# Optimization experiments

Measured on AMD Instinct MI355X. Metric: run time of the kernel, lower is better.

## Reference

```python
import jax, jax.numpy as jnp
import numpy as np

B, S, D, K, F = 4, 2048, 1024, 4, 4096
C_COEF = 8.0  # RG-LRU gating exponent from Griffin paper
EPS = 1e-6


def setup_inputs() -> dict:
    key = jax.random.key(0)
    ks = jax.random.split(key, 12)
    def n(k, shape, scale=1.0):
        return jax.random.normal(k, shape, dtype=jnp.float32) * scale
    sd = 1.0 / np.sqrt(D)
    return {
        "x": n(ks[0], (B, S, D)),
        "velocity": n(ks[1], (B, S, D), 0.1),
        "pre_norm_w": jnp.ones((D,), jnp.float32),
        "conv_kernel": n(ks[2], (D, K), 0.3),   # depthwise causal conv weights
        "conv_bias": jnp.zeros((D,), jnp.float32),
        "W_gate": n(ks[3], (D, D), sd),
        "W_a": n(ks[4], (D, D), sd),
        "lam": n(ks[5], (D,)),
        "W_out": n(ks[6], (2 * D, D), 1.0 / np.sqrt(2 * D)),
        "b_out": jnp.zeros((D,), jnp.float32),
        "log_beta": n(ks[7], (D,), 0.5),
        "ffn_norm_w": jnp.ones((D,), jnp.float32),
        "W_ff1": n(ks[8], (D, F), sd),
        "b_ff1": jnp.zeros((F,), jnp.float32),
        "W_ff2": n(ks[9], (F, D), 1.0 / np.sqrt(F)),
        "b_ff2": jnp.zeros((D,), jnp.float32),
    }


def _rmsnorm(x, w):
    # matches: rsqrt(x.float().pow(2).mean(-1, keepdim=True) + 1e-6); cast back; * weight
    xf = x.astype(jnp.float32)
    rms = jax.lax.rsqrt(jnp.mean(xf * xf, axis=-1, keepdims=True) + EPS)
    return (xf * rms).astype(x.dtype) * w


def _causal_dwconv(x, kernel, bias):
    # y[b,t,d] = bias[d] + sum_k kernel[d,k] * x[b,t-k,d]  (causal depthwise)
    k_taps = kernel.shape[1]
    s = x.shape[1]
    pad = jnp.pad(x, ((0, 0), (k_taps - 1, 0), (0, 0)))
    out = bias
    for k in range(k_taps):  # tiny fixed loop over kernel taps
        out = out + pad[:, k_taps - 1 - k : k_taps - 1 - k + s, :] * kernel[:, k]
    return out


def _griffin_scan(x, W_gate, W_a, lam):
    # RG-LRU: h_t = a_t * h_{t-1} + sqrt(1 - a_t^2) * (i_t * x_t)
    gate = jax.nn.sigmoid(jnp.einsum("bsd,de->bse", x, W_gate))
    log_a = -C_COEF * jax.nn.softplus(lam) * jax.nn.sigmoid(
        jnp.einsum("bsd,de->bse", x, W_a)
    )  # [B,S,D], log_a <= 0
    a = jnp.exp(log_a)
    u = jnp.sqrt(jnp.maximum(1.0 - a * a, 0.0)) * (gate * x)

    def step(h, au):
        a_t, u_t = au
        h = a_t * h + u_t
        return h, h

    a_t = jnp.moveaxis(a, 1, 0)  # [S,B,D]
    u_t = jnp.moveaxis(u, 1, 0)
    h0 = jnp.zeros_like(a_t[0])
    _, hs = jax.lax.scan(step, h0, (a_t, u_t))
    return jnp.moveaxis(hs, 0, 1)  # [B,S,D]


def reference(x, velocity, pre_norm_w, conv_kernel, conv_bias, W_gate, W_a, lam,
              W_out, b_out, log_beta, ffn_norm_w, W_ff1, b_ff1, W_ff2, b_ff2):
    x_norm = _rmsnorm(x, pre_norm_w)
    conv_out = _causal_dwconv(x_norm, conv_kernel, conv_bias)
    griffin_out = _griffin_scan(x_norm, W_gate, W_a, lam)
    mixer_out = jnp.concatenate([conv_out, griffin_out], axis=-1) @ W_out + b_out
    beta = jax.nn.sigmoid(log_beta)
    velocity = beta * velocity + mixer_out
    x = x + velocity
    normed = _rmsnorm(x, ffn_norm_w)
    ffn = jax.nn.gelu(normed @ W_ff1 + b_ff1) @ W_ff2 + b_ff2
    return (x + ffn, velocity)
```

## Files before the change

kernel.cpp:

```cpp
#include <hip/hip_runtime.h>

static constexpr int Bb = 4;
static constexpr int Ss = 2048;
static constexpr int Dd = 1024;
static constexpr int Ff = 4096;
static constexpr int Mm = Bb * Ss;
static constexpr size_t ND = (size_t)Mm * Dd;
static constexpr int CH = 32;
static constexpr int CL = Ss / CH;

typedef __attribute__((ext_vector_type(8))) short short8;
typedef __attribute__((ext_vector_type(4))) float floatx4;

__device__ __forceinline__ unsigned f2bf(float f) {
  unsigned u = __builtin_bit_cast(unsigned, f);
  return (u + 0x7FFFu + ((u >> 16) & 1u)) >> 16;
}
__device__ __forceinline__ float bf2f(unsigned bits) {
  return __builtin_bit_cast(float, bits << 16);
}
__device__ __forceinline__ void gload_lds16(const void* g, void* lds) {
  __builtin_amdgcn_global_load_lds((const __attribute__((address_space(1))) void*)g,
                                   (__attribute__((address_space(3))) void*)lds,
                                   16, 0, 0);
}
__device__ __forceinline__ float fsig(float x) {
  return __builtin_amdgcn_rcpf(1.0f + __expf(-x));
}
__device__ __forceinline__ float fgelu(float v) {
  float z = 1.5957691216057308f * fmaf(0.044715f * v, v * v, v);
  return v * __builtin_amdgcn_rcpf(1.0f + __expf(-z));
}

__global__ __launch_bounds__(256) void wconv_k(const float* __restrict__ W,
                                               unsigned short* __restrict__ WT,
                                               int K, int N) {
  __shared__ float tile[32][33];
  int tx = threadIdx.x & 31, ty = threadIdx.x >> 5;
  int bx = blockIdx.x * 32, by = blockIdx.y * 32;
#pragma unroll
  for (int i = 0; i < 32; i += 8)
    tile[ty + i][tx] = W[(size_t)(by + ty + i) * N + bx + tx];
  __syncthreads();
#pragma unroll
  for (int i = 0; i < 32; i += 8)
    WT[(size_t)(bx + ty + i) * K + by + tx] = (unsigned short)f2bf(tile[tx][ty + i]);
}

__global__ __launch_bounds__(256) void rmsnorm_bf_k(const float* __restrict__ x,
                                                    const float* __restrict__ w,
                                                    unsigned short* __restrict__ out) {
  int row = blockIdx.x;
  const float4* xr = (const float4*)(x + (size_t)row * Dd);
  int t = threadIdx.x;
  float4 v = xr[t];
  float ss = v.x * v.x + v.y * v.y + v.z * v.z + v.w * v.w;
#pragma unroll
  for (int off = 32; off > 0; off >>= 1) ss += __shfl_down(ss, off, 64);
  __shared__ float sb[4];
  if ((t & 63) == 0) sb[t >> 6] = ss;
  __syncthreads();
  float tot = sb[0] + sb[1] + sb[2] + sb[3];
  float sc = rsqrtf(tot * (1.0f / (float)Dd) + 1e-6f);
  float4 wv = ((const float4*)w)[t];
  unsigned lo = f2bf(v.x * sc * wv.x) | (f2bf(v.y * sc * wv.y) << 16);
  unsigned hi = f2bf(v.z * sc * wv.z) | (f2bf(v.w * sc * wv.w) << 16);
  *(uint2*)(out + (size_t)row * Dd + t * 4) = make_uint2(lo, hi);
}

__global__ __launch_bounds__(256) void conv_k(const unsigned short* __restrict__ xn,
                                              const float* __restrict__ kern,
                                              const float* __restrict__ bias,
                                              unsigned short* __restrict__ outC) {
  size_t q = (size_t)blockIdx.x * 256 + threadIdx.x;
  size_t i = q * 4;
  int d = (int)(i & (Dd - 1));
  int m = (int)(i >> 10);
  int t = m & (Ss - 1);
  float acc[4];
#pragma unroll
  for (int j = 0; j < 4; j++) acc[j] = bias[d + j];
#pragma unroll
  for (int k = 0; k < 4; k++) {
    if (t >= k) {
      uint2 xv = *(const uint2*)(xn + i - (size_t)k * Dd);
      float x0 = bf2f(xv.x & 0xFFFF), x1 = bf2f(xv.x >> 16);
      float x2 = bf2f(xv.y & 0xFFFF), x3 = bf2f(xv.y >> 16);
      acc[0] = fmaf(kern[(d + 0) * 4 + k], x0, acc[0]);
      acc[1] = fmaf(kern[(d + 1) * 4 + k], x1, acc[1]);
      acc[2] = fmaf(kern[(d + 2) * 4 + k], x2, acc[2]);
      acc[3] = fmaf(kern[(d + 3) * 4 + k], x3, acc[3]);
    }
  }
  unsigned lo = f2bf(acc[0]) | (f2bf(acc[1]) << 16);
  unsigned hi = f2bf(acc[2]) | (f2bf(acc[3]) << 16);
  *(uint2*)(outC + (size_t)m * (2 * Dd) + d) = make_uint2(lo, hi);
}

template <int MODE>
__global__ __launch_bounds__(512, 2) void bgemm3_k(const unsigned short* __restrict__ A,
                                                   const unsigned short* __restrict__ BT,
                                                   void* __restrict__ Cout,
                                                   int M, int N, int K,
                                                   const float* __restrict__ bias,
                                                   const float* __restrict__ extra,
                                                   const float* __restrict__ vel_in,
                                                   const float* __restrict__ x_in,
                                                   const float* __restrict__ log_beta,
                                                   float* __restrict__ vel_out) {
  __shared__ unsigned short LA[2][256 * 64];
  __shared__ unsigned short LB[2][256 * 64];
  const int tid = threadIdx.x;
  const int wid = tid >> 6, lane = tid & 63;
  const int wm = wid >> 2, wn = wid & 3;
  const int r = lane & 15, quad = lane >> 4, r7 = lane & 7;

  const int gx = gridDim.x;
  int id = blockIdx.y * gx + blockIdx.x;
  const int nwg = gx * gridDim.y;
  id = (id & 7) * (nwg >> 3) + (id >> 3);
  const int bm = (id / gx) * 256, bn = (id % gx) * 256;
  const int NIT = K >> 7;

  const int lrow = lane >> 3;
  const int sblk = (lane & 7) ^ lrow;
  const unsigned short* AsrcB = A  + (size_t)(bm + lrow) * K + sblk * 8;
  const unsigned short* BsrcB = BT + (size_t)(bn + lrow) * K + sblk * 8;

  const int aB = wm * 8192 + r * 64;
  const int bB = wn * 4096 + r * 64;
  const int kq0 = (quad ^ r7) * 8;
  const int kq1 = ((4 + quad) ^ r7) * 8;

  floatx4 acc[8][4];
#pragma unroll
  for (int i = 0; i < 8; i++)
#pragma unroll
    for (int j = 0; j < 4; j++) acc[i][j] = (floatx4){0.f, 0.f, 0.f, 0.f};

#define STG_A(bq, k0, h, s)                                                           \
  gload_lds16(AsrcB + (size_t)((h) * 128 + (s) * 64 + wid * 8) * K + (k0),            \
              (void*)&LA[bq][((h) * 128 + (s) * 64 + wid * 8) * 64])
#define STG_B(bq, k0, h, s)                                                           \
  gload_lds16(BsrcB + (size_t)((h) * 128 + (s) * 64 + wid * 8) * K + (k0),            \
              (void*)&LB[bq][((h) * 128 + (s) * 64 + wid * 8) * 64])
#define RDA(il, IH, buf)                                                              \
  aF[il][0] = *(const short8*)&LA[buf][aB + (IH) * 4096 + (il) * 1024 + kq0];         \
  aF[il][1] = *(const short8*)&LA[buf][aB + (IH) * 4096 + (il) * 1024 + kq1]
#define RDB(BF, jl, jg, buf)                                                          \
  BF[jl][0] = *(const short8*)&LB[buf][bB + (jg) * 1024 + kq0];                       \
  BF[jl][1] = *(const short8*)&LB[buf][bB + (jg) * 1024 + kq1]
#define MM2(il, jl, BF, IH, JH)                                                       \
  acc[(IH) * 4 + (il)][(JH) * 2 + (jl)] = __builtin_amdgcn_mfma_f32_16x16x32_bf16(    \
      BF[jl][0], aF[il][0], acc[(IH) * 4 + (il)][(JH) * 2 + (jl)], 0, 0, 0);          \
  acc[(IH) * 4 + (il)][(JH) * 2 + (jl)] = __builtin_amdgcn_mfma_f32_16x16x32_bf16(    \
      BF[jl][1], aF[il][1], acc[(IH) * 4 + (il)][(JH) * 2 + (jl)], 0, 0, 0)
#define MQUAD(BF, IH, JH)                                                             \
  MM2(0, 0, BF, IH, JH); MM2(0, 1, BF, IH, JH); MM2(1, 0, BF, IH, JH);                \
  MM2(1, 1, BF, IH, JH); MM2(2, 0, BF, IH, JH); MM2(2, 1, BF, IH, JH);                \
  MM2(3, 0, BF, IH, JH); MM2(3, 1, BF, IH, JH)
#define BAR() __builtin_amdgcn_s_barrier()
#define LGK0()                                                                        \
  asm volatile("s_waitcnt lgkmcnt(0)" ::: "memory");                                  \
  __builtin_amdgcn_sched_barrier(0)
#define PRIO(x) __builtin_amdgcn_s_setprio(x)

  STG_A(0, 0, 0, 0); STG_A(0, 0, 0, 1); STG_A(0, 0, 1, 0); STG_A(0, 0, 1, 1);
  STG_B(0, 0, 0, 0); STG_B(0, 0, 0, 1); STG_B(0, 0, 1, 0); STG_B(0, 0, 1, 1);
  STG_B(1, 64, 0, 0); STG_B(1, 64, 0, 1); STG_B(1, 64, 1, 0); STG_B(1, 64, 1, 1);
  asm volatile("s_waitcnt vmcnt(4)" ::: "memory");
  BAR();
  __builtin_amdgcn_sched_barrier(0);

  for (int it = 0; it < NIT; ++it) {
    const int T = 2 * it;
    const int pf = (it + 1 < NIT);
    const int kA1 = (T + 1) << 6;
    const int k2 = (T + 2) << 6, k3 = (T + 3) << 6;
    short8 aF[4][2], b0[2][2], b1[2][2];

    STG_A(1, kA1, 0, 0); STG_A(1, kA1, 0, 1);
    RDA(0, 0, 0); RDA(1, 0, 0); RDA(2, 0, 0); RDA(3, 0, 0);
    RDB(b0, 0, 0, 0); RDB(b0, 1, 1, 0);
    BAR(); LGK0();
    PRIO(1); MQUAD(b0, 0, 0); PRIO(0);
    BAR();

    STG_A(1, kA1, 1, 0); STG_A(1, kA1, 1, 1);
    RDB(b1, 0, 2, 0); RDB(b1, 1, 3, 0);
    BAR(); LGK0();
    PRIO(1); MQUAD(b1, 0, 1); PRIO(0);
    BAR();

    if (pf) { STG_B(0, k2, 0, 0); STG_B(0, k2, 0, 1); }
    RDA(0, 1, 0); RDA(1, 1, 0); RDA(2, 1, 0); RDA(3, 1, 0);
    BAR(); LGK0();
    PRIO(1); MQUAD(b0, 1, 0); PRIO(0);
    BAR();

    if (pf) { STG_B(0, k2, 1, 0); STG_B(0, k2, 1, 1); }
    BAR();
    PRIO(1); MQUAD(b1, 1, 1); PRIO(0);
    if (pf) asm volatile("s_waitcnt vmcnt(4)" ::: "memory");
    else    asm volatile("s_waitcnt vmcnt(0)" ::: "memory");
    BAR();
    __builtin_amdgcn_sched_barrier(0);

    if (pf) { STG_A(0, k2, 0, 0); STG_A(0, k2, 0, 1); }
    RDA(0, 0, 1); RDA(1, 0, 1); RDA(2, 0, 1); RDA(3, 0, 1);
    RDB(b0, 0, 0, 1); RDB(b0, 1, 1, 1);
    BAR(); LGK0();
    PRIO(1); MQUAD(b0, 0, 0); PRIO(0);
    BAR();

    if (pf) { STG_A(0, k2, 1, 0); STG_A(0, k2, 1, 1); }
    RDB(b1, 0, 2, 1); RDB(b1, 1, 3, 1);
    BAR(); LGK0();
    PRIO(1); MQUAD(b1, 0, 1); PRIO(0);
    BAR();

    if (pf) { STG_B(1, k3, 0, 0); STG_B(1, k3, 0, 1); }
    RDA(0, 1, 1); RDA(1, 1, 1); RDA(2, 1, 1); RDA(3, 1, 1);
    BAR(); LGK0();
    PRIO(1); MQUAD(b0, 1, 0); PRIO(0);
    BAR();

    if (pf) { STG_B(1, k3, 1, 0); STG_B(1, k3, 1, 1); }
    BAR();
    PRIO(1); MQUAD(b1, 1, 1); PRIO(0);
    if (pf) {
      asm volatile("s_waitcnt vmcnt(4)" ::: "memory");
      BAR();
      __builtin_amdgcn_sched_barrier(0);
    }
  }
#undef STG_A
#undef STG_B
#undef RDA
#undef RDB
#undef MM2
#undef MQUAD

#pragma unroll
  for (int i = 0; i < 8; i++) {
    int rowg = bm + wm * 128 + i * 16 + r;
#pragma unroll
    for (int j = 0; j < 4; j++) {
      int colg = bn + wn * 64 + j * 16 + quad * 4;
      size_t idx = (size_t)rowg * N + colg;
      float v0 = acc[i][j][0], v1 = acc[i][j][1], v2 = acc[i][j][2], v3 = acc[i][j][3];
      if (MODE & 1) {
        float4 bv = *(const float4*)(bias + colg);
        v0 += bv.x; v1 += bv.y; v2 += bv.z; v3 += bv.w;
      }
      if (MODE & 2) {
        v0 = fgelu(v0); v1 = fgelu(v1); v2 = fgelu(v2); v3 = fgelu(v3);
      }
      if (MODE & 4) {
        float4 ev = *(const float4*)(extra + idx);
        v0 += ev.x; v1 += ev.y; v2 += ev.z; v3 += ev.w;
      }
      if (MODE & 16) {
        float4 lb = *(const float4*)(log_beta + colg);
        float4 vi = *(const float4*)(vel_in + idx);
        float4 xi = *(const float4*)(x_in + idx);
        float4 vn;
        vn.x = fmaf(fsig(lb.x), vi.x, v0);
        vn.y = fmaf(fsig(lb.y), vi.y, v1);
        vn.z = fmaf(fsig(lb.z), vi.z, v2);
        vn.w = fmaf(fsig(lb.w), vi.w, v3);
        *(float4*)(vel_out + idx) = vn;
        v0 = xi.x + vn.x; v1 = xi.y + vn.y; v2 = xi.z + vn.z; v3 = xi.w + vn.w;
      }
      if (MODE & 8) {
        uint2 pk;
        pk.x = f2bf(v0) | (f2bf(v1) << 16);
        pk.y = f2bf(v2) | (f2bf(v3) << 16);
        *(uint2*)((unsigned short*)Cout + idx) = pk;
      } else {
        float4 o; o.x = v0; o.y = v1; o.z = v2; o.w = v3;
        *(float4*)((float*)Cout + idx) = o;
      }
    }
  }
}

template <int MODE>
__global__ __launch_bounds__(512, 2) void bgemm4_k(const unsigned short* __restrict__ A,
                                                   const unsigned short* __restrict__ BT,
                                                   void* __restrict__ Cout,
                                                   int M, int N, int K,
                                                   const float* __restrict__ bias,
                                                   const float* __restrict__ extra,
                                                   const float* __restrict__ vel_in,
                                                   const float* __restrict__ x_in,
                                                   const float* __restrict__ log_beta,
                                                   float* __restrict__ vel_out) {
  __shared__ unsigned short LA[3][256 * 64];
  __shared__ unsigned short LB[2][128 * 64];
  const int tid = threadIdx.x;
  const int wid = tid >> 6, lane = tid & 63;
  const int wm = wid >> 1, wn = wid & 1;
  const int r = lane & 15, quad = lane >> 4, r7 = lane & 7;

  const int gx = gridDim.x;
  int id = blockIdx.y * gx + blockIdx.x;
  const int nwg = gx * gridDim.y;
  id = (id & 7) * (nwg >> 3) + (id >> 3);
  const int bm = (id / gx) * 256, bn = (id % gx) * 128;
  const int NIT = K >> 7;

  const int lrow = lane >> 3;
  const int sblk = (lane & 7) ^ lrow;
  const unsigned short* AsrcB = A  + (size_t)(bm + lrow) * K + sblk * 8;
  const unsigned short* BsrcB = BT + (size_t)(bn + lrow) * K + sblk * 8;

  unsigned short* ALDS = &LA[0][0];
  unsigned short* B0 = &LB[0][0];
  unsigned short* B1 = &LB[1][0];

  const int aB = wm * 4096 + r * 64;
  const int bB = wn * 4096 + r * 64;
  const int kq0 = (quad ^ r7) * 8;
  const int kq1 = ((4 + quad) ^ r7) * 8;

  floatx4 acc[4][4];
#pragma unroll
  for (int i = 0; i < 4; i++)
#pragma unroll
    for (int j = 0; j < 4; j++) acc[i][j] = (floatx4){0.f, 0.f, 0.f, 0.f};

#define STG_A6(dst, k0, h, s)                                                         \
  gload_lds16(AsrcB + (size_t)((h) * 128 + (s) * 64 + wid * 8) * K + (k0),            \
              (void*)((dst) + ((h) * 128 + (s) * 64 + wid * 8) * 64))
#define STG_B6(dst, k0, s)                                                            \
  gload_lds16(BsrcB + (size_t)((s) * 64 + wid * 8) * K + (k0),                        \
              (void*)((dst) + ((s) * 64 + wid * 8) * 64))
#define RDA6(src, IH)                                                                 \
  aF[0][0] = *(const short8*)((src) + aB + (IH) * 2048 + kq0);                        \
  aF[0][1] = *(const short8*)((src) + aB + (IH) * 2048 + kq1);                        \
  aF[1][0] = *(const short8*)((src) + aB + (IH) * 2048 + 1024 + kq0);                 \
  aF[1][1] = *(const short8*)((src) + aB + (IH) * 2048 + 1024 + kq1)
#define RDB6(BF, src, JH)                                                             \
  BF[0][0] = *(const short8*)((src) + bB + (JH) * 2048 + kq0);                        \
  BF[0][1] = *(const short8*)((src) + bB + (JH) * 2048 + kq1);                        \
  BF[1][0] = *(const short8*)((src) + bB + (JH) * 2048 + 1024 + kq0);                 \
  BF[1][1] = *(const short8*)((src) + bB + (JH) * 2048 + 1024 + kq1)
#define MM26(il, jl, BF, IH, JH)                                                      \
  acc[(IH) * 2 + (il)][(JH) * 2 + (jl)] = __builtin_amdgcn_mfma_f32_16x16x32_bf16(    \
      BF[jl][0], aF[il][0], acc[(IH) * 2 + (il)][(JH) * 2 + (jl)], 0, 0, 0);          \
  acc[(IH) * 2 + (il)][(JH) * 2 + (jl)] = __builtin_amdgcn_mfma_f32_16x16x32_bf16(    \
      BF[jl][1], aF[il][1], acc[(IH) * 2 + (il)][(JH) * 2 + (jl)], 0, 0, 0)
#define MQ6(BF, IH, JH)                                                               \
  MM26(0, 0, BF, IH, JH); MM26(0, 1, BF, IH, JH);                                     \
  MM26(1, 0, BF, IH, JH); MM26(1, 1, BF, IH, JH)

  STG_A6(ALDS, 0, 0, 0); STG_A6(ALDS, 0, 0, 1); STG_A6(ALDS, 0, 1, 0); STG_A6(ALDS, 0, 1, 1);
  STG_B6(B0, 0, 0); STG_B6(B0, 0, 1);
  STG_A6(ALDS + 16384, 64, 0, 0); STG_A6(ALDS + 16384, 64, 0, 1);
  STG_A6(ALDS + 16384, 64, 1, 0); STG_A6(ALDS + 16384, 64, 1, 1);
  STG_B6(B1, 64, 0); STG_B6(B1, 64, 1);
  asm volatile("s_waitcnt vmcnt(6)" ::: "memory");
  BAR();
  __builtin_amdgcn_sched_barrier(0);

  int p = 0;
  for (int it = 0; it < NIT; ++it) {
    const int T = 2 * it;
    const int pf = (it + 1 < NIT);
    const int k2 = (T + 2) << 6, k3 = (T + 3) << 6;
    const int pn = (p == 2) ? 0 : p + 1;
    const int p2 = (pn == 2) ? 0 : pn + 1;
    unsigned short* Acur = ALDS + p * 16384;
    unsigned short* Anxt = ALDS + pn * 16384;
    unsigned short* Asg2 = ALDS + p2 * 16384;
    short8 aF[2][2], bR0[2][2], bR1[2][2];

    if (pf) { STG_A6(Asg2, k2, 0, 0); STG_A6(Asg2, k2, 0, 1); }
    RDA6(Acur, 0); RDB6(bR0, B0, 0); RDB6(bR1, B0, 1);
    BAR(); LGK0();
    PRIO(1); MQ6(bR0, 0, 0); MQ6(bR1, 0, 1); PRIO(0);
    BAR();

    if (pf) { STG_A6(Asg2, k2, 1, 0); STG_A6(Asg2, k2, 1, 1); STG_B6(B0, k2, 0); }
    RDA6(Acur, 1);
    BAR(); LGK0();
    PRIO(1); MQ6(bR0, 1, 0); MQ6(bR1, 1, 1); PRIO(0);
    if (pf) asm volatile("s_waitcnt vmcnt(5)" ::: "memory");
    else    asm volatile("s_waitcnt vmcnt(0)" ::: "memory");
    BAR();
    __builtin_amdgcn_sched_barrier(0);

    if (pf) { STG_B6(B0, k2, 1); STG_A6(Acur, k3, 0, 0); STG_A6(Acur, k3, 0, 1); }
    RDA6(Anxt, 0); RDB6(bR0, B1, 0); RDB6(bR1, B1, 1);
    BAR(); LGK0();
    PRIO(1); MQ6(bR0, 0, 0); MQ6(bR1, 0, 1); PRIO(0);
    BAR();

    if (pf) { STG_A6(Acur, k3, 1, 0); STG_A6(Acur, k3, 1, 1);
              STG_B6(B1, k3, 0); STG_B6(B1, k3, 1); }
    RDA6(Anxt, 1);
    BAR(); LGK0();
    PRIO(1); MQ6(bR0, 1, 0); MQ6(bR1, 1, 1); PRIO(0);
    if (pf) {
      asm volatile("s_waitcnt vmcnt(6)" ::: "memory");
      BAR();
      __builtin_amdgcn_sched_barrier(0);
    }
    p = p2;
  }
#undef STG_A6
#undef STG_B6
#undef RDA6
#undef RDB6
#undef MM26
#undef MQ6
#undef BAR
#undef LGK0
#undef PRIO

#pragma unroll
  for (int i = 0; i < 4; i++) {
    int rowg = bm + wm * 64 + i * 16 + r;
#pragma unroll
    for (int j = 0; j < 4; j++) {
      int colg = bn + wn * 64 + j * 16 + quad * 4;
      size_t idx = (size_t)rowg * N + colg;
      float v0 = acc[i][j][0], v1 = acc[i][j][1], v2 = acc[i][j][2], v3 = acc[i][j][3];
      if (MODE & 1) {
        float4 bv = *(const float4*)(bias + colg);
        v0 += bv.x; v1 += bv.y; v2 += bv.z; v3 += bv.w;
      }
      if (MODE & 2) {
        v0 = fgelu(v0); v1 = fgelu(v1); v2 = fgelu(v2); v3 = fgelu(v3);
      }
      if (MODE & 4) {
        float4 ev = *(const float4*)(extra + idx);
        v0 += ev.x; v1 += ev.y; v2 += ev.z; v3 += ev.w;
      }
      if (MODE & 16) {
        float4 lb = *(const float4*)(log_beta + colg);
        float4 vi = *(const float4*)(vel_in + idx);
        float4 xi = *(const float4*)(x_in + idx);
        float4 vn;
        vn.x = fmaf(fsig(lb.x), vi.x, v0);
        vn.y = fmaf(fsig(lb.y), vi.y, v1);
        vn.z = fmaf(fsig(lb.z), vi.z, v2);
        vn.w = fmaf(fsig(lb.w), vi.w, v3);
        *(float4*)(vel_out + idx) = vn;
        v0 = xi.x + vn.x; v1 = xi.y + vn.y; v2 = xi.z + vn.z; v3 = xi.w + vn.w;
      }
      if (MODE & 8) {
        uint2 pk;
        pk.x = f2bf(v0) | (f2bf(v1) << 16);
        pk.y = f2bf(v2) | (f2bf(v3) << 16);
        *(uint2*)((unsigned short*)Cout + idx) = pk;
      } else {
        float4 o; o.x = v0; o.y = v1; o.z = v2; o.w = v3;
        *(float4*)((float*)Cout + idx) = o;
      }
    }
  }
}

__global__ __launch_bounds__(256) void scan_p1(const unsigned short* __restrict__ gapre,
                                               const unsigned short* __restrict__ xn,
                                               const float* __restrict__ lam,
                                               unsigned short* __restrict__ ub,
                                               float* __restrict__ carryA,
                                               float* __restrict__ carryH) {
  int g = blockIdx.x * 256 + threadIdx.x;
  int e = g & (Dd - 1);
  int bc = g >> 10;
  int b = bc & 3;
  int c = bc >> 2;
  float l = lam[e];
  float sp = fmaxf(l, 0.0f) + log1pf(__expf(-fabsf(l)));
  float m8sp = -8.0f * sp;
  size_t m0 = (size_t)b * Ss + (size_t)c * CL;
  float A = 1.0f, h = 0.0f;
#pragma unroll 4
  for (int t = 0; t < CL; t++) {
    size_t m = m0 + t;
    float gp = bf2f(gapre[m * 2048 + e]);
    float ap = bf2f(gapre[m * 2048 + 1024 + e]);
    float xv = bf2f(xn[m * Dd + e]);
    float a = __expf(m8sp * fsig(ap));
    float u = sqrtf(fmaxf(1.0f - a * a, 0.0f)) * fsig(gp) * xv;
    ub[m * Dd + e] = (unsigned short)f2bf(u);
    A *= a;
    h = fmaf(a, h, u);
  }
  carryA[c * 4096 + b * 1024 + e] = A;
  carryH[c * 4096 + b * 1024 + e] = h;
}

__global__ __launch_bounds__(256) void scan_p2(const float* __restrict__ carryA,
                                               const float* __restrict__ carryH,
                                               float* __restrict__ init) {
  int ch = blockIdx.x * 256 + threadIdx.x;
  float H = 0.0f;
#pragma unroll
  for (int c = 0; c < CH; c++) {
    init[c * 4096 + ch] = H;
    H = fmaf(carryA[c * 4096 + ch], H, carryH[c * 4096 + ch]);
  }
}

__global__ __launch_bounds__(256) void scan_p3(const unsigned short* __restrict__ gapre,
                                               const unsigned short* __restrict__ ub,
                                               const float* __restrict__ lam,
                                               const float* __restrict__ init,
                                               unsigned short* __restrict__ outC) {
  int g = blockIdx.x * 256 + threadIdx.x;
  int e = g & (Dd - 1);
  int bc = g >> 10;
  int b = bc & 3;
  int c = bc >> 2;
  float l = lam[e];
  float sp = fmaxf(l, 0.0f) + log1pf(__expf(-fabsf(l)));
  float m8sp = -8.0f * sp;
  size_t m0 = (size_t)b * Ss + (size_t)c * CL;
  float h = init[c * 4096 + b * 1024 + e];
#pragma unroll 4
  for (int t = 0; t < CL; t++) {
    size_t m = m0 + t;
    float ap = bf2f(gapre[m * 2048 + 1024 + e]);
    float a = __expf(m8sp * fsig(ap));
    float u = bf2f(ub[m * Dd + e]);
    h = fmaf(a, h, u);
    outC[m * (2 * Dd) + Dd + e] = (unsigned short)f2bf(h);
  }
}

extern "C" void kernel_launch(void* const* d_in, const int* in_sizes, int n_in,
                              void* d_out, int out_size, void* d_ws, size_t ws_size,
                              hipStream_t stream) {
  const float* x        = (const float*)d_in[0];
  const float* velocity = (const float*)d_in[1];
  const float* pre_w    = (const float*)d_in[2];
  const float* conv_w   = (const float*)d_in[3];
  const float* conv_b   = (const float*)d_in[4];
  const float* W_gate   = (const float*)d_in[5];
  const float* W_a      = (const float*)d_in[6];
  const float* lam      = (const float*)d_in[7];
  const float* W_out    = (const float*)d_in[8];
  const float* b_out    = (const float*)d_in[9];
  const float* log_beta = (const float*)d_in[10];
  const float* ffn_w    = (const float*)d_in[11];
  const float* W_ff1    = (const float*)d_in[12];
  const float* b_ff1    = (const float*)d_in[13];
  const float* W_ff2    = (const float*)d_in[14];
  const float* b_ff2    = (const float*)d_in[15];

  float* out0 = (float*)d_out;
  float* out1 = out0 + ND;

  const size_t MB = 1024 * 1024;
  char* ws = (char*)d_ws;
  unsigned short* WgaT  = (unsigned short*)ws;
  unsigned short* WoT   = WgaT + (size_t)2 * 1024 * 1024;
  unsigned short* Wf1T  = WoT + (size_t)2 * 1024 * 1024;
  unsigned short* Wf2T  = Wf1T + (size_t)4 * 1024 * 1024;
  float*          mixer = (float*)(ws + 24 * MB);
  float*          carA  = (float*)(ws + 24 * MB);
  float*          carH  = (float*)(ws + 24 * MB + 512 * 1024);
  float*          initb = (float*)(ws + 25 * MB);
  unsigned short* conc  = (unsigned short*)(ws + 56 * MB);
  unsigned short* gapre = (unsigned short*)(ws + 88 * MB);
  unsigned short* xnbf  = (unsigned short*)(ws + 120 * MB);
  unsigned short* ubf   = (unsigned short*)(ws + 136 * MB);
  unsigned short* midbf = (unsigned short*)(ws + 88 * MB);
  unsigned short* nrmbf = (unsigned short*)(ws + 56 * MB);

  const int EB = 256;
  const int egrid4 = (int)(ND / 4 / EB);

  wconv_k<<<dim3(32, 32),  256, 0, stream>>>(W_gate, WgaT, 1024, 1024);
  wconv_k<<<dim3(32, 32),  256, 0, stream>>>(W_a,    WgaT + (size_t)1024 * 1024, 1024, 1024);
  wconv_k<<<dim3(32, 64),  256, 0, stream>>>(W_out,  WoT, 2048, 1024);
  wconv_k<<<dim3(128, 32), 256, 0, stream>>>(W_ff1,  Wf1T, 1024, 4096);
  wconv_k<<<dim3(32, 128), 256, 0, stream>>>(W_ff2,  Wf2T, 4096, 1024);
  rmsnorm_bf_k<<<Mm, 256, 0, stream>>>(x, pre_w, xnbf);
  conv_k<<<egrid4, EB, 0, stream>>>(xnbf, conv_w, conv_b, conc);
  bgemm3_k<8><<<dim3(8, 32), 512, 0, stream>>>(xnbf, WgaT, gapre, Mm, 2048, 1024,
      nullptr, nullptr, nullptr, nullptr, nullptr, nullptr);
  scan_p1<<<512, 256, 0, stream>>>(gapre, xnbf, lam, ubf, carA, carH);
  scan_p2<<<16, 256, 0, stream>>>(carA, carH, initb);
  scan_p3<<<512, 256, 0, stream>>>(gapre, ubf, lam, initb, conc);
  bgemm4_k<1 | 16><<<dim3(8, 32), 512, 0, stream>>>(conc, WoT, mixer, Mm, 1024, 2048,
      b_out, nullptr, velocity, x, log_beta, out1);
  rmsnorm_bf_k<<<Mm, 256, 0, stream>>>(mixer, ffn_w, nrmbf);
  bgemm3_k<1 | 2 | 8><<<dim3(16, 32), 512, 0, stream>>>(nrmbf, Wf1T, midbf, Mm, 4096, 1024,
      b_ff1, nullptr, nullptr, nullptr, nullptr, nullptr);
  bgemm4_k<1 | 4><<<dim3(8, 32), 512, 0, stream>>>(midbf, Wf2T, out0, Mm, 1024, 4096,
      b_ff2, mixer, nullptr, nullptr, nullptr, nullptr);
}
```

Baseline: 616.8 us.

## Split GEMM main-loop into four finer load/MFMA phases per k-tile

Restructures the bf16 MFMA GEMM main loop so each 64-wide k-step runs as four phases instead of two. Each phase does a smaller LDS read (A half or one B half), a slice of global-to-LDS prefetch, and one 4x-MFMA quad, so loads and matrix work interleave more finely. The triple-buffered A tile now rotates by swapping pointers at the end of each iteration instead of recomputing modular indices. The intent is to shorten register live ranges and hide LDS and global latency better. The cost is twice as many workgroup barriers and changed vmcnt wait counts, which could add stalls.

```diff
diff --git a/kernel.cpp b/kernel.cpp
--- a/kernel.cpp
+++ b/kernel.cpp
@@ -315,7 +315,9 @@
   const unsigned short* AsrcB = A  + (size_t)(bm + lrow) * K + sblk * 8;
   const unsigned short* BsrcB = BT + (size_t)(bn + lrow) * K + sblk * 8;
 
-  unsigned short* ALDS = &LA[0][0];
+  unsigned short* a0 = &LA[0][0];
+  unsigned short* a1 = &LA[1][0];
+  unsigned short* a2 = &LA[2][0];
   unsigned short* B0 = &LB[0][0];
   unsigned short* B1 = &LB[1][0];
 
@@ -330,91 +332,106 @@
 #pragma unroll
     for (int j = 0; j < 4; j++) acc[i][j] = (floatx4){0.f, 0.f, 0.f, 0.f};
 
-#define STG_A6(dst, k0, h, s)                                                         \
+#define STG_A7(dst, k0, h, s)                                                         \
   gload_lds16(AsrcB + (size_t)((h) * 128 + (s) * 64 + wid * 8) * K + (k0),            \
               (void*)((dst) + ((h) * 128 + (s) * 64 + wid * 8) * 64))
-#define STG_B6(dst, k0, s)                                                            \
+#define STG_B7(dst, k0, s)                                                            \
   gload_lds16(BsrcB + (size_t)((s) * 64 + wid * 8) * K + (k0),                        \
               (void*)((dst) + ((s) * 64 + wid * 8) * 64))
-#define RDA6(src, IH)                                                                 \
+#define RDA7(src, IH)                                                                 \
   aF[0][0] = *(const short8*)((src) + aB + (IH) * 2048 + kq0);                        \
   aF[0][1] = *(const short8*)((src) + aB + (IH) * 2048 + kq1);                        \
   aF[1][0] = *(const short8*)((src) + aB + (IH) * 2048 + 1024 + kq0);                 \
   aF[1][1] = *(const short8*)((src) + aB + (IH) * 2048 + 1024 + kq1)
-#define RDB6(BF, src, JH)                                                             \
+#define RDB7(BF, src, JH)                                                             \
   BF[0][0] = *(const short8*)((src) + bB + (JH) * 2048 + kq0);                        \
   BF[0][1] = *(const short8*)((src) + bB + (JH) * 2048 + kq1);                        \
   BF[1][0] = *(const short8*)((src) + bB + (JH) * 2048 + 1024 + kq0);                 \
   BF[1][1] = *(const short8*)((src) + bB + (JH) * 2048 + 1024 + kq1)
-#define MM26(il, jl, BF, IH, JH)                                                      \
+#define MM27(il, jl, BF, IH, JH)                                                      \
   acc[(IH) * 2 + (il)][(JH) * 2 + (jl)] = __builtin_amdgcn_mfma_f32_16x16x32_bf16(    \
       BF[jl][0], aF[il][0], acc[(IH) * 2 + (il)][(JH) * 2 + (jl)], 0, 0, 0);          \
   acc[(IH) * 2 + (il)][(JH) * 2 + (jl)] = __builtin_amdgcn_mfma_f32_16x16x32_bf16(    \
       BF[jl][1], aF[il][1], acc[(IH) * 2 + (il)][(JH) * 2 + (jl)], 0, 0, 0)
-#define MQ6(BF, IH, JH)                                                               \
-  MM26(0, 0, BF, IH, JH); MM26(0, 1, BF, IH, JH);                                     \
-  MM26(1, 0, BF, IH, JH); MM26(1, 1, BF, IH, JH)
-
-  STG_A6(ALDS, 0, 0, 0); STG_A6(ALDS, 0, 0, 1); STG_A6(ALDS, 0, 1, 0); STG_A6(ALDS, 0, 1, 1);
-  STG_B6(B0, 0, 0); STG_B6(B0, 0, 1);
-  STG_A6(ALDS + 16384, 64, 0, 0); STG_A6(ALDS + 16384, 64, 0, 1);
-  STG_A6(ALDS + 16384, 64, 1, 0); STG_A6(ALDS + 16384, 64, 1, 1);
-  STG_B6(B1, 64, 0); STG_B6(B1, 64, 1);
+#define MQ7(BF, IH, JH)                                                               \
+  MM27(0, 0, BF, IH, JH); MM27(0, 1, BF, IH, JH);                                     \
+  MM27(1, 0, BF, IH, JH); MM27(1, 1, BF, IH, JH)
+
+  STG_A7(a0, 0, 0, 0); STG_A7(a0, 0, 0, 1); STG_A7(a0, 0, 1, 0); STG_A7(a0, 0, 1, 1);
+  STG_B7(B0, 0, 0); STG_B7(B0, 0, 1);
+  STG_A7(a1, 64, 0, 0); STG_A7(a1, 64, 0, 1); STG_A7(a1, 64, 1, 0); STG_A7(a1, 64, 1, 1);
+  STG_B7(B1, 64, 0); STG_B7(B1, 64, 1);
   asm volatile("s_waitcnt vmcnt(6)" ::: "memory");
   BAR();
   __builtin_amdgcn_sched_barrier(0);
 
-  int p = 0;
   for (int it = 0; it < NIT; ++it) {
     const int T = 2 * it;
     const int pf = (it + 1 < NIT);
     const int k2 = (T + 2) << 6, k3 = (T + 3) << 6;
-    const int pn = (p == 2) ? 0 : p + 1;
-    const int p2 = (pn == 2) ? 0 : pn + 1;
-    unsigned short* Acur = ALDS + p * 16384;
-    unsigned short* Anxt = ALDS + pn * 16384;
-    unsigned short* Asg2 = ALDS + p2 * 16384;
-    short8 aF[2][2], bR0[2][2], bR1[2][2];
-
-    if (pf) { STG_A6(Asg2, k2, 0, 0); STG_A6(Asg2, k2, 0, 1); }
-    RDA6(Acur, 0); RDB6(bR0, B0, 0); RDB6(bR1, B0, 1);
-    BAR(); LGK0();
-    PRIO(1); MQ6(bR0, 0, 0); MQ6(bR1, 0, 1); PRIO(0);
-    BAR();
-
-    if (pf) { STG_A6(Asg2, k2, 1, 0); STG_A6(Asg2, k2, 1, 1); STG_B6(B0, k2, 0); }
-    RDA6(Acur, 1);
-    BAR(); LGK0();
-    PRIO(1); MQ6(bR0, 1, 0); MQ6(bR1, 1, 1); PRIO(0);
-    if (pf) asm volatile("s_waitcnt vmcnt(5)" ::: "memory");
+    short8 aF[2][2], b0f[2][2], b1f[2][2];
+
+    if (pf) { STG_A7(a2, k2, 0, 0); STG_A7(a2, k2, 0, 1); }
+    RDA7(a0, 0); RDB7(b0f, B0, 0);
+    BAR(); LGK0();
+    PRIO(1); MQ7(b0f, 0, 0); PRIO(0);
+    BAR();
+
+    if (pf) { STG_A7(a2, k2, 1, 0); STG_A7(a2, k2, 1, 1); }
+    RDB7(b1f, B0, 1);
+    BAR(); LGK0();
+    PRIO(1); MQ7(b1f, 0, 1); PRIO(0);
+    BAR();
+
+    if (pf) STG_B7(B0, k2, 0);
+    RDA7(a0, 1);
+    BAR(); LGK0();
+    PRIO(1); MQ7(b0f, 1, 0); PRIO(0);
+    BAR();
+
+    if (pf) STG_B7(B0, k2, 1);
+    BAR();
+    PRIO(1); MQ7(b1f, 1, 1); PRIO(0);
+    if (pf) asm volatile("s_waitcnt vmcnt(6)" ::: "memory");
     else    asm volatile("s_waitcnt vmcnt(0)" ::: "memory");
     BAR();
     __builtin_amdgcn_sched_barrier(0);
 
-    if (pf) { STG_B6(B0, k2, 1); STG_A6(Acur, k3, 0, 0); STG_A6(Acur, k3, 0, 1); }
-    RDA6(Anxt, 0); RDB6(bR0, B1, 0); RDB6(bR1, B1, 1);
-    BAR(); LGK0();
-    PRIO(1); MQ6(bR0, 0, 0); MQ6(bR1, 0, 1); PRIO(0);
-    BAR();
-
-    if (pf) { STG_A6(Acur, k3, 1, 0); STG_A6(Acur, k3, 1, 1);
-              STG_B6(B1, k3, 0); STG_B6(B1, k3, 1); }
-    RDA6(Anxt, 1);
-    BAR(); LGK0();
-    PRIO(1); MQ6(bR0, 1, 0); MQ6(bR1, 1, 1); PRIO(0);
+    if (pf) { STG_A7(a0, k3, 0, 0); STG_A7(a0, k3, 0, 1); }
+    RDA7(a1, 0); RDB7(b0f, B1, 0);
+    BAR(); LGK0();
+    PRIO(1); MQ7(b0f, 0, 0); PRIO(0);
+    BAR();
+
+    if (pf) { STG_A7(a0, k3, 1, 0); STG_A7(a0, k3, 1, 1); }
+    RDB7(b1f, B1, 1);
+    BAR(); LGK0();
+    PRIO(1); MQ7(b1f, 0, 1); PRIO(0);
+    BAR();
+
+    if (pf) STG_B7(B1, k3, 0);
+    RDA7(a1, 1);
+    BAR(); LGK0();
+    PRIO(1); MQ7(b0f, 1, 0); PRIO(0);
+    BAR();
+
+    if (pf) STG_B7(B1, k3, 1);
+    BAR();
+    PRIO(1); MQ7(b1f, 1, 1); PRIO(0);
     if (pf) {
       asm volatile("s_waitcnt vmcnt(6)" ::: "memory");
       BAR();
       __builtin_amdgcn_sched_barrier(0);
     }
-    p = p2;
-  }
-#undef STG_A6
-#undef STG_B6
-#undef RDA6
-#undef RDB6
-#undef MM26
-#undef MQ6
+
+    unsigned short* tmp = a2; a2 = a1; a1 = a0; a0 = tmp;
+  }
+#undef STG_A7
+#undef STG_B7
+#undef RDA7
+#undef RDB7
+#undef MM27
+#undef MQ7
 #undef BAR
 #undef LGK0
 #undef PRIO
```

Result: faster. 562.3 us (-8.8%).
